# Optimization experiments

Hardware: AMD Instinct MI355X
Metric: run time of the kernel (lower is better)

## Reference

```python
import jax, jax.numpy as jnp
from jax import lax
import numpy as np

MAL = 10  # max_atom_len

def _conv1d(x, w, b):
    # x: [N,C,L], w: [O,I,K], 'same' padding for K=3 (pad 1)
    pad = (w.shape[-1] - 1) // 2
    y = lax.conv_general_dilated(x, w, (1,), [(pad, pad)], dimension_numbers=('NCH', 'OIH', 'NCH'))
    return y + b[None, :, None]

def _maxpool2(x):
    return lax.reduce_window(x, -jnp.inf, lax.max, (1, 1, 2), (1, 1, 2), 'VALID')

def setup_inputs():
    key = jax.random.key(0)
    ks = jax.random.split(key, 32)
    def p(i, shape):
        return 0.05 * jax.random.normal(ks[i], shape, jnp.float32)
    bs, seq, C, L = 128, 128, 6, 20
    D, H = 64, 256
    return {
        'x': jax.random.normal(ks[0], (bs, seq, C, L), jnp.float32),
        'imu_mask': jnp.ones((bs, seq, C, L), jnp.float32),
        'imu_len': jax.random.randint(ks[1], (bs,), 1, seq + 1),
        'c1_w': p(2, (16, 6, 3)), 'c1_b': p(3, (16,)),
        'c2_w': p(4, (32, 16, 3)), 'c2_b': p(5, (32,)),
        'c3_w': p(6, (32, 32, 3)), 'c3_b': p(7, (32,)),
        'br_w': p(8, (64, D)), 'br_b': p(9, (D,)),
        'f1_w': p(10, (D, H)), 'f1_b': p(11, (H,)),
        'f2_w': p(12, (H, D)), 'f2_b': p(13, (D,)),
        'd1_w': p(14, (16, 32, 5)), 'd1_b': p(15, (32,)),
        'd2_w': p(16, (6, 32, 3)), 'd2_b': p(17, (6,)),
        'ae1_w': p(18, (32, D, 3)), 'ae1_b': p(19, (32,)),
        'ae2_w': p(20, (16, 32, 3)), 'ae2_b': p(21, (16,)),
        'ae3_w': p(22, (80, 32)), 'ae3_b': p(23, (32,)),
        'ad1_w': p(24, (32, H)), 'ad1_b': p(25, (H,)),
        'ad2_w': p(26, (H, 6 * MAL * seq)), 'ad2_b': p(27, (6 * MAL * seq,)),
    }

def reference(x, imu_mask, c1_w, c1_b, c2_w, c2_b, c3_w, c3_b, br_w, br_b,
              f1_w, f1_b, f2_w, f2_b, d1_w, d1_b, d2_w, d2_b,
              ae1_w, ae1_b, ae2_w, ae2_b, ae3_w, ae3_b,
              ad1_w, ad1_b, ad2_w, ad2_b, imu_len):
    bs, seq, C, L = x.shape
    N = bs * seq
    # --- CNN encoder: [N,6,20] -> [N,32,2] -> flat 64 ---
    h = _maxpool2(jax.nn.relu(_conv1d(x.reshape(N, C, L), c1_w, c1_b)))  # [N,16,10]
    h = _maxpool2(jax.nn.relu(_conv1d(h, c2_w, c2_b)))                   # [N,32,5]
    h = _maxpool2(jax.nn.relu(_conv1d(h, c3_w, c3_b)))                   # [N,32,2]
    cnn_out = h.reshape(N, -1)
    bridge_out = jax.nn.sigmoid(cnn_out @ br_w + br_b)  # [N,D]
    D = bridge_out.shape[1]
    # --- forecast branch ---
    forcast_in3 = bridge_out.reshape(bs, seq, D)
    shft = jnp.pad(forcast_in3, ((0, 0), (1, 0), (0, 0)))[:, :-1]  # shift right by 1
    fmask = jnp.ones((bs, seq, D), jnp.float32).at[:, 0, :].set(0.0).reshape(N, D)
    fmask = fmask * imu_mask[:, :, 0, 0].reshape(N, 1)
    forcast_in = forcast_in3.reshape(N, D)
    feat = jax.nn.relu(shft.reshape(N, D) @ f1_w + f1_b)
    forcast = feat @ f2_w + f2_b
    forcast_loss = jnp.mean(jnp.square((forcast - forcast_in) * fmask), axis=1)  # [N]
    loss2d = forcast_loss.reshape(bs, seq)
    # --- host-side segmentation (mirrors original sort/argwhere/.item() loop) ---
    scores = np.asarray(forcast_loss * fmask[:, 0])
    k = int(scores.shape[0] * 0.2)
    cutoff = float(np.sort(scores)[::-1][:k].min())
    l2 = np.asarray(loss2d)
    seg_lists = []
    for b in range(bs):
        idxs = np.nonzero(l2[b] > cutoff)[0]
        segs = []
        if idxs.shape[0] > 0:
            for i in range(idxs.shape[0] - 1):
                if int(idxs[i + 1] - idxs[i]) > MAL:
                    cur = int(idxs[i]); segs.append(cur)
                    while cur < int(idxs[i + 1]):
                        cur += MAL
                        if cur >= int(idxs[i + 1]):
                            break
                        segs.append(cur)
                else:
                    segs.append(int(idxs[i]))
            segs.append(int(idxs[-1]))
        seg_lists.append(segs)
    # --- build variable-length atoms (left-pad / left-crop to fixed widths) ---
    bridge_np = np.asarray(forcast_in3)
    x_np = np.asarray(x)
    Wtot = MAL * seq
    feats, atoms, masks = [], [], []
    for b in range(bs):
        last = 0
        for e in seg_lists[b]:
            f = bridge_np[b, last:e]  # [n,D]
            pad = MAL - f.shape[0]
            fp = np.concatenate([np.zeros((pad, D), np.float32), f], 0) if pad >= 0 else f[-pad:]
            a = x_np[b, last:e].transpose(1, 0, 2).reshape(C, -1)  # [C, n*L]
            ap = Wtot - a.shape[1]
            if ap >= 0:
                apad = np.concatenate([np.zeros((C, ap), np.float32), a], 1)
                m = np.zeros((C, Wtot), np.float32); m[:, ap:] = 1.0
            else:
                apad = a[:, -ap:]; m = np.ones((C, Wtot), np.float32)
            feats.append(fp); atoms.append(apad); masks.append(m)
            last = e
    if len(feats) == 0:  # degenerate guard
        feats = [np.zeros((MAL, D), np.float32)]
        atoms = [np.zeros((C, Wtot), np.float32)]
        masks = [np.zeros((C, Wtot), np.float32)]
    A = len(feats)
    atom_features = jnp.asarray(np.stack(feats)).swapaxes(1, 2)  # [A,D,MAL]
    imu_atoms = jnp.asarray(np.stack(atoms))                      # [A,C,Wtot]
    imu_atoms_mask = jnp.asarray(np.stack(masks))
    # --- atom encoder / decoder ---
    ha = _maxpool2(jax.nn.relu(_conv1d(atom_features, ae1_w, ae1_b)))  # [A,32,5]
    ha = jax.nn.relu(_conv1d(ha, ae2_w, ae2_b))                        # [A,16,5]
    emb = ha.reshape(A, -1) @ ae3_w + ae3_b                            # [A,32]
    hd = jax.nn.relu(emb @ ad1_w + ad1_b)
    atom_gen = (hd @ ad2_w + ad2_b).reshape(A, C, Wtot)
    # --- imu decoder: [N,16,4] -> [N,6,20] ---
    bridge_resh = bridge_out.reshape(N, 16, 4)
    # non-overlapping transpose conv (kernel=stride=5): 4 -> 20
    g = jnp.einsum('nci,cok->noik', bridge_resh, d1_w).reshape(N, 32, 20)
    g = jax.nn.relu(g + d1_b[None, :, None])
    imu_gen = _conv1d(g, d2_w, d2_b).reshape(bs, seq, C, L)
    return (imu_gen, atom_gen, imu_atoms_mask, imu_atoms, bridge_resh,
            forcast_in, forcast, fmask, forcast_loss)
```

## Files before the change

### kernel.cpp

```cpp
#include <hip/hip_runtime.h>
#include <math.h>


#define NWIN 16384
#define SEQ  128
#define BS   128
#define KSEL 3276
#define SEGSTRIDE 160
#define RECCAP 18432

typedef __attribute__((ext_vector_type(8))) short short8v;
typedef __attribute__((ext_vector_type(4))) float float4v;

__device__ inline unsigned short bf16rne(float f) {
    unsigned u = __float_as_uint(f);
    unsigned r = u + 0x7FFFu + ((u >> 16) & 1u);
    return (unsigned short)(r >> 16);
}

__global__ __launch_bounds__(256) void k_encoder(
        const float* __restrict__ x,
        const float* __restrict__ c1w, const float* __restrict__ c1b,
        const float* __restrict__ c2w, const float* __restrict__ c2b,
        const float* __restrict__ c3w, const float* __restrict__ c3b,
        const float* __restrict__ brw, const float* __restrict__ brb,
        float* __restrict__ bridge, float* __restrict__ out_resh,
        float* __restrict__ out_fin) {
    __shared__ float c1wt[288];
    __shared__ float c2wt[1536];
    __shared__ float c3wt[3072];
    __shared__ float brws[4096];
    __shared__ float c1bs[16], c2bs[32], c3bs[32], brbs[64];
    __shared__ float xs[4][128], c1s[4][160], c2s[4][160], c3s[4][64];

    int tid = threadIdx.x;
    for (int i = tid; i < 288; i += 256) {
        int oc = i / 18, r = i - oc * 18, ic = r / 3, dk = r - ic * 3;
        c1wt[(ic * 3 + dk) * 16 + oc] = c1w[i];
    }
    for (int i = tid; i < 1536; i += 256) {
        int oc = i / 48, r = i - oc * 48, ic = r / 3, dk = r - ic * 3;
        c2wt[(ic * 3 + dk) * 32 + oc] = c2w[i];
    }
    for (int i = tid; i < 3072; i += 256) {
        int oc = i / 96, r = i - oc * 96, ic = r / 3, dk = r - ic * 3;
        c3wt[(ic * 3 + dk) * 32 + oc] = c3w[i];
    }
    for (int i = tid; i < 4096; i += 256) brws[i] = brw[i];
    if (tid < 16) c1bs[tid] = c1b[tid];
    else if (tid < 48) c2bs[tid - 16] = c2b[tid - 16];
    else if (tid < 80) c3bs[tid - 48] = c3b[tid - 48];
    else if (tid < 144) brbs[tid - 80] = brb[tid - 80];

    int wv = tid >> 6, lane = tid & 63;
    int n = blockIdx.x * 4 + wv;
    const float* xr = x + (size_t)n * 120;
    if (lane < 60) ((float2*)&xs[wv][0])[lane] = ((const float2*)xr)[lane];
    __syncthreads();

    {
        int oc = lane >> 2, tg = lane & 3;
        float bb = c1bs[oc];
        float acc[3][2];
#pragma unroll
        for (int j = 0; j < 3; ++j) { acc[j][0] = bb; acc[j][1] = bb; }
        for (int ic = 0; ic < 6; ++ic) {
            float w0 = c1wt[(ic * 3 + 0) * 16 + oc];
            float w1 = c1wt[(ic * 3 + 1) * 16 + oc];
            float w2 = c1wt[(ic * 3 + 2) * 16 + oc];
            const float* ar = &xs[wv][ic * 20];
#pragma unroll
            for (int j = 0; j < 3; ++j) {
                int t = tg + 4 * j;
                if (t < 10) {
#pragma unroll
                    for (int q = 0; q < 2; ++q) {
                        int p = 2 * t + q;
                        float a0 = (p >= 1) ? ar[p - 1] : 0.f;
                        float a1 = ar[p];
                        float a2 = (p + 1 < 20) ? ar[p + 1] : 0.f;
                        acc[j][q] += a0 * w0 + a1 * w1 + a2 * w2;
                    }
                }
            }
        }
#pragma unroll
        for (int j = 0; j < 3; ++j) {
            int t = tg + 4 * j;
            if (t < 10) c1s[wv][oc * 10 + t] = fmaxf(fmaxf(acc[j][0], acc[j][1]), 0.f);
        }
    }
    __syncthreads();

    {
        int oc = lane >> 1, tg = lane & 1;
        float bb = c2bs[oc];
        float acc[3][2];
#pragma unroll
        for (int j = 0; j < 3; ++j) { acc[j][0] = bb; acc[j][1] = bb; }
        for (int ic = 0; ic < 16; ++ic) {
            float w0 = c2wt[(ic * 3 + 0) * 32 + oc];
            float w1 = c2wt[(ic * 3 + 1) * 32 + oc];
            float w2 = c2wt[(ic * 3 + 2) * 32 + oc];
            const float* ar = &c1s[wv][ic * 10];
#pragma unroll
            for (int j = 0; j < 3; ++j) {
                int t = tg + 2 * j;
                if (t < 5) {
#pragma unroll
                    for (int q = 0; q < 2; ++q) {
                        int p = 2 * t + q;
                        float a0 = (p >= 1) ? ar[p - 1] : 0.f;
                        float a1 = ar[p];
                        float a2 = (p + 1 < 10) ? ar[p + 1] : 0.f;
                        acc[j][q] += a0 * w0 + a1 * w1 + a2 * w2;
                    }
                }
            }
        }
#pragma unroll
        for (int j = 0; j < 3; ++j) {
            int t = tg + 2 * j;
            if (t < 5) c2s[wv][oc * 5 + t] = fmaxf(fmaxf(acc[j][0], acc[j][1]), 0.f);
        }
    }
    __syncthreads();

    {
        int oc = lane >> 1, tp = lane & 1;
        float bb = c3bs[oc];
        float acc0 = bb, acc1 = bb;
        for (int ic = 0; ic < 32; ++ic) {
            float w0 = c3wt[(ic * 3 + 0) * 32 + oc];
            float w1 = c3wt[(ic * 3 + 1) * 32 + oc];
            float w2 = c3wt[(ic * 3 + 2) * 32 + oc];
            const float* ar = &c2s[wv][ic * 5];
            {
                int p = 2 * tp;
                float a0 = (p >= 1) ? ar[p - 1] : 0.f;
                acc0 += a0 * w0 + ar[p] * w1 + ar[p + 1] * w2;
            }
            {
                int p = 2 * tp + 1;
                acc1 += ar[p - 1] * w0 + ar[p] * w1 + ((p + 1 < 5) ? ar[p + 1] : 0.f) * w2;
            }
        }
        c3s[wv][lane] = fmaxf(fmaxf(acc0, acc1), 0.f);
    }
    __syncthreads();

    {
        float acc = brbs[lane];
        for (int i = 0; i < 64; ++i) acc += c3s[wv][i] * brws[i * 64 + lane];
        float v = 1.f / (1.f + expf(-acc));
        size_t o = (size_t)n * 64 + lane;
        bridge[o] = v; out_resh[o] = v; out_fin[o] = v;
    }
}

__global__ __launch_bounds__(512) void k_forecast(
        const float* __restrict__ bridge,
        const float* __restrict__ w1, const float* __restrict__ b1,
        const float* __restrict__ w2, const float* __restrict__ b2,
        const float* __restrict__ imu_mask,
        float* __restrict__ out_fc, float* __restrict__ out_fmask,
        float* __restrict__ out_loss, float* __restrict__ scores) {
    __shared__ float w1s[16384];
    __shared__ float w2s[16384];
    __shared__ float b1s[256], b2s[64];
    __shared__ float fts[8][256];

    int tid = threadIdx.x;
    {
        const float4* s1 = (const float4*)w1;
        const float4* s2 = (const float4*)w2;
        float4* d1 = (float4*)w1s;
        float4* d2 = (float4*)w2s;
        for (int i = tid; i < 4096; i += 512) { d1[i] = s1[i]; d2[i] = s2[i]; }
    }
    if (tid < 256) b1s[tid] = b1[tid];
    else if (tid < 320) b2s[tid - 256] = b2[tid - 256];
    __syncthreads();

    int wv = tid >> 6, lane = tid & 63;
    int nbase = blockIdx.x * 64 + wv * 8;
#pragma unroll 1
    for (int i = 0; i < 8; ++i) {
        int n = nbase + i;
        int s = n & (SEQ - 1);
        float acc[4];
#pragma unroll
        for (int j = 0; j < 4; ++j) acc[j] = b1s[lane + 64 * j];
        if (s > 0) {
            float brv = bridge[(size_t)(n - 1) * 64 + lane];
#pragma unroll 4
            for (int d = 0; d < 64; ++d) {
                float bd = __shfl(brv, d);
#pragma unroll
                for (int j = 0; j < 4; ++j)
                    acc[j] += bd * w1s[d * 256 + lane + 64 * j];
            }
        }
#pragma unroll
        for (int j = 0; j < 4; ++j) fts[wv][lane + 64 * j] = fmaxf(acc[j], 0.f);
        float fa = b2s[lane];
#pragma unroll 8
        for (int h = 0; h < 256; ++h) fa += fts[wv][h] * w2s[h * 64 + lane];
        out_fc[(size_t)n * 64 + lane] = fa;
        float mval = (s == 0) ? 0.f : imu_mask[(size_t)n * 120];
        out_fmask[(size_t)n * 64 + lane] = mval;
        float diff = (fa - bridge[(size_t)n * 64 + lane]) * mval;
        float sq = diff * diff;
#pragma unroll
        for (int off = 32; off; off >>= 1) sq += __shfl_down(sq, off);
        if (lane == 0) {
            float loss = sq * (1.f / 64.f);
            out_loss[n] = loss;
            scores[n] = loss * mval;
        }
    }
}

__global__ __launch_bounds__(256) void k_postsel(
        const float* __restrict__ scores, const float* __restrict__ loss,
        int* __restrict__ rec_b, int* __restrict__ rec_last,
        int* __restrict__ rec_e, int* __restrict__ total_out) {
    __shared__ unsigned hist[4][256];
    __shared__ unsigned sh_prefix;
    __shared__ int sh_k;
    __shared__ int segs[BS][SEGSTRIDE];
    __shared__ int counts[BS];
    __shared__ int offs[BS + 1];
    int tid = threadIdx.x, wv = tid >> 6;
    if (tid == 0) { sh_prefix = 0u; sh_k = KSEL; }
    __syncthreads();
    for (int shift = 24; shift >= 0; shift -= 8) {
#pragma unroll
        for (int w = 0; w < 4; ++w) hist[w][tid] = 0u;
        __syncthreads();
        unsigned prefix = sh_prefix;
        unsigned pmask = (shift == 24) ? 0u : (0xFFFFFFFFu << (shift + 8));
        for (int i = tid; i < NWIN; i += 256) {
            unsigned u = __float_as_uint(scores[i]);
            if ((u & pmask) == prefix) atomicAdd(&hist[wv][(u >> shift) & 255u], 1u);
        }
        __syncthreads();
        if (tid == 0) {
            int kk = sh_k;
            for (int bin = 255; bin >= 0; --bin) {
                int c = (int)(hist[0][bin] + hist[1][bin] + hist[2][bin] + hist[3][bin]);
                if (kk <= c) { sh_prefix = prefix | ((unsigned)bin << shift); sh_k = kk; break; }
                kk -= c;
            }
        }
        __syncthreads();
    }
    float cutoff = __uint_as_float(sh_prefix);

    if (tid < BS) {
        int b = tid;
        int* my = segs[b];
        int cnt = 0, prev = 0;
        bool has = false;
        for (int s = 0; s < SEQ; ++s) {
            if (loss[b * SEQ + s] > cutoff) {
                if (has) {
                    if (s - prev > 10) {
                        my[cnt++] = prev;
                        int cur = prev;
                        while (cur < s) {
                            cur += 10;
                            if (cur >= s) break;
                            my[cnt++] = cur;
                        }
                    } else {
                        my[cnt++] = prev;
                    }
                }
                has = true; prev = s;
            }
        }
        if (has) my[cnt++] = prev;
        counts[b] = cnt;
    }
    __syncthreads();
    if (tid == 0) {
        int acc = 0;
        for (int b = 0; b < BS; ++b) { offs[b] = acc; acc += counts[b]; }
        offs[BS] = acc;
        *total_out = acc;
        if (acc == 0) { rec_b[0] = 0; rec_last[0] = 0; rec_e[0] = 0; }
    }
    __syncthreads();
    if (tid < BS) {
        int b = tid;
        int o = offs[b], c = counts[b];
        for (int j = 0; j < c; ++j) {
            int idx = o + j;
            if (idx >= RECCAP) break;
            rec_b[idx] = b;
            rec_last[idx] = (j > 0) ? segs[b][j - 1] : 0;
            rec_e[idx] = segs[b][j];
        }
    }
}

__global__ void k_gather_atoms(const int* __restrict__ rec_b, const int* __restrict__ rec_last,
                               const int* __restrict__ rec_e, const float* __restrict__ x,
                               float* __restrict__ out_atoms, float* __restrict__ out_mask, int A) {
    int gid = blockIdx.x * blockDim.x + threadIdx.x;
    if (gid >= A * 7680) return;
    int a = gid / 7680, rem = gid % 7680, c = rem / 1280, wcol = rem % 1280;
    int b = rec_b[a], last = rec_last[a], e = rec_e[a];
    int W = (e - last) * 20;
    int sc = wcol - (1280 - W);
    float v = 0.f, m = 0.f;
    if (sc >= 0 && sc < W) {
        int t = sc / 20, l = sc % 20;
        v = x[((b * SEQ + last + t) * 6 + c) * 20 + l];
        m = 1.f;
    }
    out_atoms[gid] = v;
    out_mask[gid] = m;
}

__global__ __launch_bounds__(256) void k_ae2(
        const int* __restrict__ rec_b, const int* __restrict__ rec_last,
        const int* __restrict__ rec_e, const float* __restrict__ bridge,
        const float* __restrict__ ae1w, const float* __restrict__ ae1b,
        const float* __restrict__ ae2w, const float* __restrict__ ae2b,
        const float* __restrict__ ae3w, const float* __restrict__ ae3b,
        const float* __restrict__ ad1w, const float* __restrict__ ad1b,
        unsigned short* __restrict__ hd, int A) {
    __shared__ float ae1wt[6144];
    __shared__ float ae2wt[1536];
    __shared__ float ae3ws[2560];
    __shared__ float ae1bs[32], ae2bs[16], ae3bs[32];
    __shared__ float af_s[8][640];
    __shared__ float c1p[8][160];
    __shared__ float h2s[8][80];
    __shared__ float embs[32][8];

    int tid = threadIdx.x;
    int a0 = blockIdx.x * 8;

    for (int i = tid; i < 6144; i += 256) {
        int o = i / 192, r = i - o * 192, ic = r / 3, dk = r - ic * 3;
        ae1wt[(ic * 3 + dk) * 32 + o] = ae1w[i];
    }
    for (int i = tid; i < 1536; i += 256) {
        int c = i / 96, r = i - c * 96, ic = r / 3, dk = r - ic * 3;
        ae2wt[(ic * 3 + dk) * 16 + c] = ae2w[i];
    }
    for (int i = tid; i < 2560; i += 256) ae3ws[i] = ae3w[i];
    if (tid < 32) ae1bs[tid] = ae1b[tid];
    else if (tid < 48) ae2bs[tid - 32] = ae2b[tid - 32];
    else if (tid < 80) ae3bs[tid - 48] = ae3b[tid - 48];

    int wv = tid >> 6, lane = tid & 63;
#pragma unroll
    for (int sg = 0; sg < 2; ++sg) {
        int seg = wv * 2 + sg;
        int ac = a0 + seg; if (ac > A - 1) ac = A - 1;
        int b = rec_b[ac], last = rec_last[ac], e = rec_e[ac];
#pragma unroll
        for (int r = 0; r < 10; ++r) {
            int src = e - 10 + r;
            float v = (src >= last) ? bridge[(size_t)(b * SEQ + src) * 64 + lane] : 0.f;
            af_s[seg][lane * 10 + r] = v;
        }
    }
    __syncthreads();

    {
        int seg = wv * 2 + (lane >> 5);
        int o = lane & 31;
        const float* afl = af_s[seg];
        float bb = ae1bs[o];
        float acc[10];
#pragma unroll
        for (int p = 0; p < 10; ++p) acc[p] = bb;
        for (int ic = 0; ic < 64; ++ic) {
            float av[10];
#pragma unroll
            for (int r = 0; r < 10; ++r) av[r] = afl[ic * 10 + r];
            float w0 = ae1wt[(ic * 3 + 0) * 32 + o];
            float w1 = ae1wt[(ic * 3 + 1) * 32 + o];
            float w2 = ae1wt[(ic * 3 + 2) * 32 + o];
            acc[0] += av[0] * w1 + av[1] * w2;
#pragma unroll
            for (int p = 1; p < 9; ++p)
                acc[p] += av[p - 1] * w0 + av[p] * w1 + av[p + 1] * w2;
            acc[9] += av[8] * w0 + av[9] * w1;
        }
#pragma unroll
        for (int t = 0; t < 5; ++t)
            c1p[seg][o * 5 + t] = fmaxf(fmaxf(acc[2 * t], acc[2 * t + 1]), 0.f);
    }
    __syncthreads();

    {
        int seg = wv * 2 + (lane >> 5);
        int c = (lane & 31) >> 1, th = lane & 1;
        const float* cp = c1p[seg];
        float bb = ae2bs[c];
        float acc2[3] = {bb, bb, bb};
        for (int ic = 0; ic < 32; ++ic) {
            float m[5];
#pragma unroll
            for (int t = 0; t < 5; ++t) m[t] = cp[ic * 5 + t];
            float w0 = ae2wt[(ic * 3 + 0) * 16 + c];
            float w1 = ae2wt[(ic * 3 + 1) * 16 + c];
            float w2 = ae2wt[(ic * 3 + 2) * 16 + c];
#pragma unroll
            for (int j = 0; j < 3; ++j) {
                int t = th + 2 * j;
                if (t < 5) {
                    float am1 = (t > 0) ? m[t - 1] : 0.f;
                    float ap1 = (t < 4) ? m[t + 1] : 0.f;
                    acc2[j] += am1 * w0 + m[t] * w1 + ap1 * w2;
                }
            }
        }
#pragma unroll
        for (int j = 0; j < 3; ++j) {
            int t = th + 2 * j;
            if (t < 5) h2s[seg][c * 5 + t] = fmaxf(acc2[j], 0.f);
        }
    }
    __syncthreads();

    {
        int seg = wv * 2 + (lane >> 5);
        int o = lane & 31;
        float acc = ae3bs[o];
        const float* hh = h2s[seg];
        for (int i = 0; i < 80; ++i) acc += hh[i] * ae3ws[i * 32 + o];
        embs[o][seg] = acc;
    }
    __syncthreads();

    {
        int idx = tid;
        float bb = ad1b[idx];
        float acc[8];
#pragma unroll
        for (int s = 0; s < 8; ++s) acc[s] = bb;
        for (int o = 0; o < 32; ++o) {
            float wq = ad1w[o * 256 + idx];
#pragma unroll
            for (int s = 0; s < 8; ++s) acc[s] += embs[o][s] * wq;
        }
#pragma unroll
        for (int s = 0; s < 8; ++s) {
            int a = a0 + s;
            if (a < A) hd[(size_t)a * 256 + idx] = bf16rne(fmaxf(acc[s], 0.f));
        }
    }
}

__global__ __launch_bounds__(256) void k_wtrans(const float* __restrict__ w,
                                                unsigned short* __restrict__ wbT) {
    __shared__ float tile[64][65];
    int n0 = blockIdx.x * 64, k0 = blockIdx.y * 64;
    int tid = threadIdx.x;
    int c = tid & 63;
    for (int r = tid >> 6; r < 64; r += 4)
        tile[r][c] = w[(size_t)(k0 + r) * 7680 + n0 + c];
    __syncthreads();
    int n = tid >> 4, kq = (tid & 15) * 4;
    for (int nn = n; nn < 64; nn += 16) {
        unsigned p0 = (unsigned)bf16rne(tile[kq + 0][nn]) |
                      ((unsigned)bf16rne(tile[kq + 1][nn]) << 16);
        unsigned p1 = (unsigned)bf16rne(tile[kq + 2][nn]) |
                      ((unsigned)bf16rne(tile[kq + 3][nn]) << 16);
        unsigned* dst = (unsigned*)&wbT[(size_t)(n0 + nn) * 256 + k0 + kq];
        dst[0] = p0; dst[1] = p1;
    }
}

#define LSTR 264
__global__ __launch_bounds__(256) void k_ad2m(const unsigned short* __restrict__ hdb,
                                              const unsigned short* __restrict__ wbT,
                                              const float* __restrict__ bias,
                                              float* __restrict__ out, int A) {
    __shared__ unsigned short wt[64 * LSTR];
    int tid = threadIdx.x;
    int m0 = blockIdx.x * 64;
    int n0 = blockIdx.y * 64;

    {
        const short8v* src = (const short8v*)(wbT + (size_t)n0 * 256);
#pragma unroll
        for (int i = 0; i < 8; ++i) {
            int flat = tid + 256 * i;
            int row = flat >> 5, ch = flat & 31;
            short8v v = src[flat];
            *(short8v*)&wt[row * LSTR + ch * 8] = v;
        }
    }
    __syncthreads();

    int wv = tid >> 6, lane = tid & 63;
    int rc = lane & 15;
    int koff = (lane >> 4) * 8;
    float4v acc[4];
#pragma unroll
    for (int i = 0; i < 4; ++i) acc[i] = (float4v){0.f, 0.f, 0.f, 0.f};

    const short* ha = (const short*)hdb + (size_t)(m0 + wv * 16 + rc) * 256 + koff;
#pragma unroll
    for (int s = 0; s < 8; ++s) {
        short8v a = *(const short8v*)(ha + s * 32);
#pragma unroll
        for (int nt = 0; nt < 4; ++nt) {
            short8v b = *(const short8v*)((const short*)&wt[(nt * 16 + rc) * LSTR + s * 32 + koff]);
            acc[nt] = __builtin_amdgcn_mfma_f32_16x16x32_bf16(a, b, acc[nt], 0, 0, 0);
        }
    }

    int quad = lane >> 4;
#pragma unroll
    for (int nt = 0; nt < 4; ++nt) {
        int n = n0 + nt * 16 + rc;
        float bb = bias[n];
#pragma unroll
        for (int r = 0; r < 4; ++r) {
            int m = m0 + wv * 16 + quad * 4 + r;
            if (m < A) out[(size_t)m * 7680 + n] = acc[nt][r] + bb;
        }
    }
}

__global__ __launch_bounds__(256) void k_decoder(const float* __restrict__ bridge,
                          const float* __restrict__ d1w, const float* __restrict__ d1b,
                          const float* __restrict__ d2w, const float* __restrict__ d2b,
                          float* __restrict__ out) {
    __shared__ float d1wt[16 * 5 * 33];
    __shared__ float d2wt[576];
    __shared__ float d1bs[32], d2bs[8];
    __shared__ float brs[4][64];
    __shared__ float gs[4][640];
    int tid = threadIdx.x;
    for (int i = tid; i < 2560; i += 256) {
        int c = i / 160, r = i - c * 160, o = r / 5, kk = r - o * 5;
        d1wt[(c * 5 + kk) * 33 + o] = d1w[i];
    }
    for (int i = tid; i < 576; i += 256) {
        int oc = i / 96, r = i - oc * 96, ic = r / 3, dk = r - ic * 3;
        d2wt[(ic * 3 + dk) * 6 + oc] = d2w[i];
    }
    if (tid < 32) d1bs[tid] = d1b[tid];
    else if (tid < 38) d2bs[tid - 32] = d2b[tid - 32];
    int wv = tid >> 6, lane = tid & 63;
    int n = blockIdx.x * 4 + wv;
    brs[wv][lane] = bridge[(size_t)n * 64 + lane];
    __syncthreads();
    for (int idx = lane; idx < 640; idx += 64) {
        int o = idx / 20, p = idx - o * 20, i = p / 5, kk = p - i * 5;
        float acc = d1bs[o];
#pragma unroll
        for (int c = 0; c < 16; ++c) acc += brs[wv][c * 4 + i] * d1wt[(c * 5 + kk) * 33 + o];
        gs[wv][idx] = fmaxf(acc, 0.f);
    }
    __syncthreads();
    for (int idx = lane; idx < 120; idx += 64) {
        int oc = idx / 20, t = idx - oc * 20;
        float acc = d2bs[oc];
        for (int ic = 0; ic < 32; ++ic) {
            const float* gr = &gs[wv][ic * 20];
            float a0 = (t >= 1) ? gr[t - 1] : 0.f;
            float a1 = gr[t];
            float a2 = (t + 1 < 20) ? gr[t + 1] : 0.f;
            acc += a0 * d2wt[(ic * 3 + 0) * 6 + oc]
                 + a1 * d2wt[(ic * 3 + 1) * 6 + oc]
                 + a2 * d2wt[(ic * 3 + 2) * 6 + oc];
        }
        out[(size_t)n * 120 + idx] = acc;
    }
}

extern "C" void kernel_launch(void* const* d_in, const int* in_sizes, int n_in,
                              void* d_out, int out_size, void* d_ws, size_t ws_size,
                              hipStream_t stream) {
    const float* x        = (const float*)d_in[0];
    const float* imu_mask = (const float*)d_in[1];
    const float* c1_w = (const float*)d_in[3];
    const float* c1_b = (const float*)d_in[4];
    const float* c2_w = (const float*)d_in[5];
    const float* c2_b = (const float*)d_in[6];
    const float* c3_w = (const float*)d_in[7];
    const float* c3_b = (const float*)d_in[8];
    const float* br_w = (const float*)d_in[9];
    const float* br_b = (const float*)d_in[10];
    const float* f1_w = (const float*)d_in[11];
    const float* f1_b = (const float*)d_in[12];
    const float* f2_w = (const float*)d_in[13];
    const float* f2_b = (const float*)d_in[14];
    const float* d1_w = (const float*)d_in[15];
    const float* d1_b = (const float*)d_in[16];
    const float* d2_w = (const float*)d_in[17];
    const float* d2_b = (const float*)d_in[18];
    const float* ae1_w = (const float*)d_in[19];
    const float* ae1_b = (const float*)d_in[20];
    const float* ae2_w = (const float*)d_in[21];
    const float* ae2_b = (const float*)d_in[22];
    const float* ae3_w = (const float*)d_in[23];
    const float* ae3_b = (const float*)d_in[24];
    const float* ad1_w = (const float*)d_in[25];
    const float* ad1_b = (const float*)d_in[26];
    const float* ad2_w = (const float*)d_in[27];
    const float* ad2_b = (const float*)d_in[28];

    int A = (out_size - 6176768) / 23040;
    if (A < 1) A = 1;

    float* out = (float*)d_out;
    size_t o_imu_gen  = 0;
    size_t o_atom_gen = 1966080;
    size_t o_mask     = o_atom_gen + (size_t)A * 7680;
    size_t o_atoms    = o_mask + (size_t)A * 7680;
    size_t o_resh     = o_atoms + (size_t)A * 7680;
    size_t o_fin      = o_resh + 1048576;
    size_t o_fc       = o_fin + 1048576;
    size_t o_fmask    = o_fc + 1048576;
    size_t o_loss     = o_fmask + 1048576;

    float* wsf = (float*)d_ws;
    int*   wsi = (int*)d_ws;
    const size_t W_BRIDGE = 0;
    const size_t W_FEAT   = W_BRIDGE + 1048576;
    const size_t W_SCORES = W_FEAT + 4194304;
    const size_t W_CUTOFF = W_SCORES + 16384;
    const size_t MW       = W_CUTOFF + 64;
    int* counts   = wsi + MW;
    int* total    = wsi + MW + 128;
    int* segs     = wsi + MW + 192;
    int* rec_b    = wsi + MW + 192 + BS * SEGSTRIDE;
    int* rec_last = rec_b + RECCAP;
    int* rec_e    = rec_last + RECCAP;
    size_t HD_OFF = MW + 192 + BS * SEGSTRIDE + 3 * RECCAP;
    unsigned short* hd  = (unsigned short*)(wsf + HD_OFF);
    unsigned short* wbT = (unsigned short*)(wsf + HD_OFF + (size_t)RECCAP * 128);
    (void)counts; (void)segs;

    hipMemsetAsync(rec_b, 0, 3 * RECCAP * sizeof(int), stream);

    const int T = 256;
    dim3 gt(120, 4);
    k_wtrans<<<gt, 256, 0, stream>>>(ad2_w, wbT);
    k_encoder<<<NWIN / 4, 256, 0, stream>>>(x, c1_w, c1_b, c2_w, c2_b, c3_w, c3_b,
                                            br_w, br_b, wsf + W_BRIDGE,
                                            out + o_resh, out + o_fin);
    k_forecast<<<NWIN / 64, 512, 0, stream>>>(wsf + W_BRIDGE, f1_w, f1_b, f2_w, f2_b,
                                              imu_mask, out + o_fc, out + o_fmask,
                                              out + o_loss, wsf + W_SCORES);
    k_postsel<<<1, 256, 0, stream>>>(wsf + W_SCORES, out + o_loss,
                                     rec_b, rec_last, rec_e, total);
    k_gather_atoms<<<(A * 7680 + T - 1) / T, T, 0, stream>>>(rec_b, rec_last, rec_e, x,
                                                             out + o_atoms, out + o_mask, A);
    k_ae2<<<(A + 7) / 8, 256, 0, stream>>>(rec_b, rec_last, rec_e, wsf + W_BRIDGE,
                                           ae1_w, ae1_b, ae2_w, ae2_b, ae3_w, ae3_b,
                                           ad1_w, ad1_b, hd, A);
    dim3 g2((A + 63) / 64, 120);
    k_ad2m<<<g2, 256, 0, stream>>>(hd, wbT, ad2_b, out + o_atom_gen, A);
    k_decoder<<<NWIN / 4, 256, 0, stream>>>(wsf + W_BRIDGE, d1_w, d1_b, d2_w, d2_b,
                                            out + o_imu_gen);
}
```

Measured before the change: 893.1 us.

## Batch forecast MLP over four windows, vectorize atom gather, enlarge ad2 GEMM tiles

The forecast kernel now handles four windows per wave together. It reads a permuted w1 as float4 and broadcasts activations with readlane instead of shuffles and an LDS staging buffer, so each weight load is reused four times. The atom gather kernel now gives each thread one 20-float timestep row, copied with float4 loads and stores, instead of one scalar element per thread. The ad2 GEMM uses 512-thread blocks covering 128 rows, which halves how often the weight tile is staged. The costs are higher register pressure in the forecast kernel and fewer blocks for the GEMM.

Result: slower. 1.127 ms (+26.2%).

```diff
diff --git a/kernel.cpp b/kernel.cpp
--- a/kernel.cpp
+++ b/kernel.cpp
@@ -16,6 +16,10 @@
     unsigned u = __float_as_uint(f);
     unsigned r = u + 0x7FFFu + ((u >> 16) & 1u);
     return (unsigned short)(r >> 16);
+}
+
+__device__ inline float rdlane(float v, int l) {
+    return __uint_as_float(__builtin_amdgcn_readlane(__float_as_uint(v), l));
 }
 
 __global__ __launch_bounds__(256) void k_encoder(
@@ -165,18 +169,19 @@
         const float* __restrict__ imu_mask,
         float* __restrict__ out_fc, float* __restrict__ out_fmask,
         float* __restrict__ out_loss, float* __restrict__ scores) {
-    __shared__ float w1s[16384];
+    __shared__ float w1p[16384];
     __shared__ float w2s[16384];
     __shared__ float b1s[256], b2s[64];
-    __shared__ float fts[8][256];
 
     int tid = threadIdx.x;
-    {
-        const float4* s1 = (const float4*)w1;
+    for (int i = tid; i < 16384; i += 512) {
+        int d = i >> 8, h = i & 255;
+        w1p[d * 256 + ((h & 63) << 2) + (h >> 6)] = w1[i];
+    }
+    {
         const float4* s2 = (const float4*)w2;
-        float4* d1 = (float4*)w1s;
         float4* d2 = (float4*)w2s;
-        for (int i = tid; i < 4096; i += 512) { d1[i] = s1[i]; d2[i] = s2[i]; }
+        for (int i = tid; i < 4096; i += 512) d2[i] = s2[i];
     }
     if (tid < 256) b1s[tid] = b1[tid];
     else if (tid < 320) b2s[tid - 256] = b2[tid - 256];
@@ -185,38 +190,64 @@
     int wv = tid >> 6, lane = tid & 63;
     int nbase = blockIdx.x * 64 + wv * 8;
 #pragma unroll 1
-    for (int i = 0; i < 8; ++i) {
-        int n = nbase + i;
-        int s = n & (SEQ - 1);
-        float acc[4];
-#pragma unroll
-        for (int j = 0; j < 4; ++j) acc[j] = b1s[lane + 64 * j];
-        if (s > 0) {
-            float brv = bridge[(size_t)(n - 1) * 64 + lane];
-#pragma unroll 4
-            for (int d = 0; d < 64; ++d) {
-                float bd = __shfl(brv, d);
-#pragma unroll
-                for (int j = 0; j < 4; ++j)
-                    acc[j] += bd * w1s[d * 256 + lane + 64 * j];
-            }
-        }
-#pragma unroll
-        for (int j = 0; j < 4; ++j) fts[wv][lane + 64 * j] = fmaxf(acc[j], 0.f);
-        float fa = b2s[lane];
-#pragma unroll 8
-        for (int h = 0; h < 256; ++h) fa += fts[wv][h] * w2s[h * 64 + lane];
-        out_fc[(size_t)n * 64 + lane] = fa;
-        float mval = (s == 0) ? 0.f : imu_mask[(size_t)n * 120];
-        out_fmask[(size_t)n * 64 + lane] = mval;
-        float diff = (fa - bridge[(size_t)n * 64 + lane]) * mval;
-        float sq = diff * diff;
-#pragma unroll
-        for (int off = 32; off; off >>= 1) sq += __shfl_down(sq, off);
-        if (lane == 0) {
-            float loss = sq * (1.f / 64.f);
-            out_loss[n] = loss;
-            scores[n] = loss * mval;
+    for (int p = 0; p < 2; ++p) {
+        int n0 = nbase + p * 4;
+        float brv[4], acc1[4][4];
+#pragma unroll
+        for (int wi = 0; wi < 4; ++wi) {
+            int n = n0 + wi;
+            int s = n & (SEQ - 1);
+            brv[wi] = (s > 0) ? bridge[(size_t)(n - 1) * 64 + lane] : 0.f;
+#pragma unroll
+            for (int j = 0; j < 4; ++j) acc1[wi][j] = b1s[lane + 64 * j];
+        }
+#pragma unroll
+        for (int d = 0; d < 64; ++d) {
+            float4 wq = *(const float4*)&w1p[d * 256 + (lane << 2)];
+#pragma unroll
+            for (int wi = 0; wi < 4; ++wi) {
+                float bd = rdlane(brv[wi], d);
+                acc1[wi][0] += bd * wq.x;
+                acc1[wi][1] += bd * wq.y;
+                acc1[wi][2] += bd * wq.z;
+                acc1[wi][3] += bd * wq.w;
+            }
+        }
+        float ft[4][4];
+#pragma unroll
+        for (int wi = 0; wi < 4; ++wi)
+#pragma unroll
+            for (int j = 0; j < 4; ++j) ft[wi][j] = fmaxf(acc1[wi][j], 0.f);
+
+        float fa[4];
+#pragma unroll
+        for (int wi = 0; wi < 4; ++wi) fa[wi] = b2s[lane];
+#pragma unroll
+        for (int j = 0; j < 4; ++j) {
+#pragma unroll
+            for (int src = 0; src < 64; ++src) {
+                float w2v = w2s[((j << 6) + src) * 64 + lane];
+#pragma unroll
+                for (int wi = 0; wi < 4; ++wi)
+                    fa[wi] += rdlane(ft[wi][j], src) * w2v;
+            }
+        }
+#pragma unroll
+        for (int wi = 0; wi < 4; ++wi) {
+            int n = n0 + wi;
+            int s = n & (SEQ - 1);
+            out_fc[(size_t)n * 64 + lane] = fa[wi];
+            float mval = (s == 0) ? 0.f : imu_mask[(size_t)n * 120];
+            out_fmask[(size_t)n * 64 + lane] = mval;
+            float diff = (fa[wi] - bridge[(size_t)n * 64 + lane]) * mval;
+            float sq = diff * diff;
+#pragma unroll
+            for (int off = 32; off; off >>= 1) sq += __shfl_down(sq, off);
+            if (lane == 0) {
+                float loss = sq * (1.f / 64.f);
+                out_loss[n] = loss;
+                scores[n] = loss * mval;
+            }
         }
     }
 }
@@ -309,19 +340,28 @@
                                const int* __restrict__ rec_e, const float* __restrict__ x,
                                float* __restrict__ out_atoms, float* __restrict__ out_mask, int A) {
     int gid = blockIdx.x * blockDim.x + threadIdx.x;
-    if (gid >= A * 7680) return;
-    int a = gid / 7680, rem = gid % 7680, c = rem / 1280, wcol = rem % 1280;
+    if (gid >= A * 384) return;
+    int a = gid / 384, rem = gid - a * 384;
+    int c = rem >> 6, k = rem & 63;
     int b = rec_b[a], last = rec_last[a], e = rec_e[a];
-    int W = (e - last) * 20;
-    int sc = wcol - (1280 - W);
-    float v = 0.f, m = 0.f;
-    if (sc >= 0 && sc < W) {
-        int t = sc / 20, l = sc % 20;
-        v = x[((b * SEQ + last + t) * 6 + c) * 20 + l];
+    int nt = e - last;
+    int t = k - (64 - nt);
+    float4 v0, v1, v2, v3, v4;
+    float m;
+    if (t >= 0 && t < nt) {
+        const float4* src = (const float4*)(x + ((size_t)((b * SEQ + last + t) * 6 + c)) * 20);
+        v0 = src[0]; v1 = src[1]; v2 = src[2]; v3 = src[3]; v4 = src[4];
         m = 1.f;
-    }
-    out_atoms[gid] = v;
-    out_mask[gid] = m;
+    } else {
+        v0 = v1 = v2 = v3 = v4 = (float4){0.f, 0.f, 0.f, 0.f};
+        m = 0.f;
+    }
+    size_t obase = (size_t)a * 7680 + c * 1280 + k * 20;
+    float4* da = (float4*)(out_atoms + obase);
+    da[0] = v0; da[1] = v1; da[2] = v2; da[3] = v3; da[4] = v4;
+    float4 mv = (float4){m, m, m, m};
+    float4* dm = (float4*)(out_mask + obase);
+    dm[0] = mv; dm[1] = mv; dm[2] = mv; dm[3] = mv; dm[4] = mv;
 }
 
 __global__ __launch_bounds__(256) void k_ae2(
@@ -480,20 +520,20 @@
 }
 
 #define LSTR 264
-__global__ __launch_bounds__(256) void k_ad2m(const unsigned short* __restrict__ hdb,
+__global__ __launch_bounds__(512) void k_ad2m(const unsigned short* __restrict__ hdb,
                                               const unsigned short* __restrict__ wbT,
                                               const float* __restrict__ bias,
                                               float* __restrict__ out, int A) {
     __shared__ unsigned short wt[64 * LSTR];
     int tid = threadIdx.x;
-    int m0 = blockIdx.x * 64;
+    int m0 = blockIdx.x * 128;
     int n0 = blockIdx.y * 64;
 
     {
         const short8v* src = (const short8v*)(wbT + (size_t)n0 * 256);
 #pragma unroll
-        for (int i = 0; i < 8; ++i) {
-            int flat = tid + 256 * i;
+        for (int i = 0; i < 4; ++i) {
+            int flat = tid + 512 * i;
             int row = flat >> 5, ch = flat & 31;
             short8v v = src[flat];
             *(short8v*)&wt[row * LSTR + ch * 8] = v;
@@ -633,16 +673,13 @@
     const size_t W_SCORES = W_FEAT + 4194304;
     const size_t W_CUTOFF = W_SCORES + 16384;
     const size_t MW       = W_CUTOFF + 64;
-    int* counts   = wsi + MW;
     int* total    = wsi + MW + 128;
-    int* segs     = wsi + MW + 192;
     int* rec_b    = wsi + MW + 192 + BS * SEGSTRIDE;
     int* rec_last = rec_b + RECCAP;
     int* rec_e    = rec_last + RECCAP;
     size_t HD_OFF = MW + 192 + BS * SEGSTRIDE + 3 * RECCAP;
     unsigned short* hd  = (unsigned short*)(wsf + HD_OFF);
     unsigned short* wbT = (unsigned short*)(wsf + HD_OFF + (size_t)RECCAP * 128);
-    (void)counts; (void)segs;
 
     hipMemsetAsync(rec_b, 0, 3 * RECCAP * sizeof(int), stream);
 
@@ -657,13 +694,13 @@
                                               out + o_loss, wsf + W_SCORES);
     k_postsel<<<1, 256, 0, stream>>>(wsf + W_SCORES, out + o_loss,
                                      rec_b, rec_last, rec_e, total);
-    k_gather_atoms<<<(A * 7680 + T - 1) / T, T, 0, stream>>>(rec_b, rec_last, rec_e, x,
-                                                             out + o_atoms, out + o_mask, A);
+    k_gather_atoms<<<(A * 384 + T - 1) / T, T, 0, stream>>>(rec_b, rec_last, rec_e, x,
+                                                            out + o_atoms, out + o_mask, A);
     k_ae2<<<(A + 7) / 8, 256, 0, stream>>>(rec_b, rec_last, rec_e, wsf + W_BRIDGE,
                                            ae1_w, ae1_b, ae2_w, ae2_b, ae3_w, ae3_b,
                                            ad1_w, ad1_b, hd, A);
-    dim3 g2((A + 63) / 64, 120);
-    k_ad2m<<<g2, 256, 0, stream>>>(hd, wbT, ad2_b, out + o_atom_gen, A);
+    dim3 g2((A + 127) / 128, 120);
+    k_ad2m<<<g2, 512, 0, stream>>>(hd, wbT, ad2_b, out + o_atom_gen, A);
     k_decoder<<<NWIN / 4, 256, 0, stream>>>(wsf + W_BRIDGE, d1_w, d1_b, d2_w, d2_b,
                                             out + o_imu_gen);
 }
```
